# Kernel tuning notes

Measured on AMD Instinct MI355X. Metric: run time of the kernel, lower is better.

Reference implementation:

```python
import jax, jax.numpy as jnp
import numpy as np

N, IN_DIM, HID, HEADS, OUT_DIM = 4096, 512, 128, 4, 64
ALPHA = 0.2
NEG_INF = -9e15  # matches torch's -9000000000000000.0 fill


def _gat_layer(adj_mask, h, W, a, concat):
    # h: [N, Fin], W: [Fin, Fout], a: [2*Fout, 1]
    Wh = h @ W                                   # [N, Fout]
    f_out = W.shape[1]
    Wh1 = Wh @ a[:f_out]                         # [N, 1]
    Wh2 = Wh @ a[f_out:]                         # [N, 1]
    e = jax.nn.leaky_relu(Wh1 + Wh2.T, ALPHA)    # [N, N] broadcast scores
    e = jnp.where(adj_mask, e, NEG_INF)
    att = jax.nn.softmax(e, axis=1)              # masked row softmax
    out = att @ Wh                               # [N, Fout] aggregate
    return jax.nn.elu(out) if concat else out


def setup_inputs() -> dict:
    key = jax.random.key(0)
    k = jax.random.split(key, 6)
    g = jax.random.randint(k[0], (N, N), 0, 2, dtype=jnp.int32)
    inputs = jax.random.normal(k[1], (N, IN_DIM), dtype=jnp.float32)
    # xavier-uniform-like scales
    s1 = np.sqrt(6.0 / (IN_DIM + HID)) * 1.414
    sa1 = np.sqrt(6.0 / (2 * HID + 1)) * 1.414
    s2 = np.sqrt(6.0 / (HID * HEADS + OUT_DIM)) * 1.414
    sa2 = np.sqrt(6.0 / (2 * OUT_DIM + 1)) * 1.414
    W1 = jax.random.uniform(k[2], (HEADS, IN_DIM, HID), jnp.float32, -s1, s1)
    a1 = jax.random.uniform(k[3], (HEADS, 2 * HID, 1), jnp.float32, -sa1, sa1)
    W2 = jax.random.uniform(k[4], (HID * HEADS, OUT_DIM), jnp.float32, -s2, s2)
    a2 = jax.random.uniform(k[5], (2 * OUT_DIM, 1), jnp.float32, -sa2, sa2)
    return {"g": g, "inputs": inputs, "W1": W1, "a1": a1, "W2": W2, "a2": a2}


def reference(g, inputs, W1, a1, W2, a2):
    adj_mask = g > 0                                              # [N, N] bool
    # layer 1: HEADS parallel heads, concat=True (elu), then concat on features
    heads_out = jax.vmap(lambda W, a: _gat_layer(adj_mask, inputs, W, a, True))(W1, a1)
    h = jnp.transpose(heads_out, (1, 0, 2)).reshape(N, HEADS * HID)  # [N, H*HID]
    # output attention layer, concat=False (no elu)
    return _gat_layer(adj_mask, h, W2, a2, False)                 # [N, OUT_DIM]
```

## Files before the change

### kernel.cpp

```cpp
#include <hip/hip_runtime.h>
#include <hip/hip_bf16.h>
#include <stdint.h>

#define NN 4096
#define KD 512
#define LOG2E 1.4426950408889634f

typedef __attribute__((ext_vector_type(8))) short short8;
typedef __attribute__((ext_vector_type(4))) float f32x4;

__device__ __forceinline__ float lrelu(float x) { return fmaxf(x, 0.2f * x); }

__device__ __forceinline__ unsigned short f2bf(float f) {
    uint32_t u = __float_as_uint(f);
    u += 0x7fff + ((u >> 16) & 1);
    return (unsigned short)(u >> 16);
}

__device__ __forceinline__ float exp2_fast(float x) {
    float r; asm("v_exp_f32 %0, %1" : "=v"(r) : "v"(x)); return r;
}

__device__ __forceinline__ uint32_t cvt_pk_bf16(float lo, float hi) {
    uint32_t r; asm("v_cvt_pk_bf16_f32 %0, %1, %2" : "=v"(r) : "v"(lo), "v"(hi)); return r;
}

__device__ __forceinline__ void glds16(const void* g, void* l) {
    __builtin_amdgcn_global_load_lds(
        (const __attribute__((address_space(1))) uint32_t*)g,
        (__attribute__((address_space(3))) uint32_t*)l, 16, 0, 0);
}

__global__ void k_bitmask(const int* __restrict__ g, uint64_t* __restrict__ bm) {
    int wave = threadIdx.x >> 6;
    int lane = threadIdx.x & 63;
    int row = blockIdx.x * 4 + wave;
    const int* grow = g + (size_t)row * NN;
    for (int w = 0; w < 64; ++w) {
        int v = grow[w * 64 + lane];
        unsigned long long m = __ballot(v > 0);
        if (lane == 0) bm[(size_t)row * 64 + w] = m;
    }
}

__global__ void k_cast(const float* __restrict__ x, unsigned short* __restrict__ y, int n4) {
    int i = blockIdx.x * 256 + threadIdx.x;
    if (i < n4) {
        float4 v = ((const float4*)x)[i];
        uint2 o;
        o.x = (uint32_t)f2bf(v.x) | ((uint32_t)f2bf(v.y) << 16);
        o.y = (uint32_t)f2bf(v.z) | ((uint32_t)f2bf(v.w) << 16);
        ((uint2*)y)[i] = o;
    }
}

__global__ __launch_bounds__(256)
void k_tc(const float* __restrict__ src, unsigned short* __restrict__ dst, int R, int C) {
    __shared__ float tile[64][65];
    int b = blockIdx.z;
    int r0 = blockIdx.x * 64, c0 = blockIdx.y * 64;
    src += (size_t)b * R * C;
    dst += (size_t)b * C * R;
    int t = threadIdx.x;
    #pragma unroll
    for (int s = 0; s < 16; ++s) {
        int idx = t + s * 256;
        int r = idx >> 6, c = idx & 63;
        tile[r][c] = src[(size_t)(r0 + r) * C + c0 + c];
    }
    __syncthreads();
    #pragma unroll
    for (int s = 0; s < 16; ++s) {
        int idx = t + s * 256;
        int r = idx >> 6, c = idx & 63;
        dst[(size_t)(c0 + r) * R + r0 + c] = f2bf(tile[c][r]);
    }
}

template <int F>
__global__ __launch_bounds__(512)
void k_gemm_fused(const unsigned short* __restrict__ Abf, const unsigned short* __restrict__ WT,
                  const float* __restrict__ avec,
                  unsigned short* __restrict__ WhT, float* __restrict__ s1g,
                  float* __restrict__ s2g, unsigned int* __restrict__ smaxKey) {
    constexpr int BM = 32, BK = 64;
    constexpr int NCF = F / 64;
    __shared__ unsigned short a_lds[2][BM * BK];
    __shared__ unsigned short b_lds[2][F * BK];
    __shared__ unsigned short t_lds[F * 40];
    __shared__ float sred[BM][2];
    int t = threadIdx.x, lane = t & 63, w = t >> 6;
    int h = blockIdx.y;
    int i0 = blockIdx.x * BM;
    const unsigned short* WTh = WT + (size_t)h * F * KD;
    int r0 = (w >> 2) * 16, c0 = (w & 3) * (F / 4);
    int krow = lane & 15, kgrp = lane >> 4;
    if (t < BM) { sred[t][0] = 0.f; sred[t][1] = 0.f; }
    f32x4 acc[NCF];
    #pragma unroll
    for (int cf = 0; cf < NCF; ++cf) acc[cf] = (f32x4){0.f, 0.f, 0.f, 0.f};

    auto stage = [&](int buf, int kt) {
        int k0 = kt * BK;
        if (w < 4) {
            int c = w * 64 + lane;
            int row = c >> 3, slot = c & 7;
            glds16(Abf + (size_t)(i0 + row) * KD + k0 + ((slot ^ (row & 7)) * 8),
                   &a_lds[buf][(w * 64) * 8]);
        }
        #pragma unroll
        for (int s = 0; s < F / 64; ++s) {
            int c = w * F + s * 64 + lane;
            int row = c >> 3, slot = c & 7;
            glds16(WTh + (size_t)row * KD + k0 + ((slot ^ (row & 7)) * 8),
                   &b_lds[buf][(w * F + s * 64) * 8]);
        }
    };

    stage(0, 0);
    __syncthreads();
    int cur = 0;
    for (int kt = 0; kt < KD / BK; ++kt) {
        int nxt = cur ^ 1;
        if (kt + 1 < KD / BK) stage(nxt, kt + 1);
        #pragma unroll
        for (int ks = 0; ks < 2; ++ks) {
            int koff = ks * 32 + kgrp * 8;
            int arow = r0 + krow;
            short8 av = *(const short8*)((const char*)&a_lds[cur][arow * BK] +
                                         ((koff * 2) ^ ((arow & 7) << 4)));
            #pragma unroll
            for (int cf = 0; cf < NCF; ++cf) {
                int brow = c0 + cf * 16 + krow;
                short8 bv = *(const short8*)((const char*)&b_lds[cur][brow * BK] +
                                             ((koff * 2) ^ ((brow & 7) << 4)));
                acc[cf] = __builtin_amdgcn_mfma_f32_16x16x32_bf16(av, bv, acc[cf], 0, 0, 0);
            }
        }
        __syncthreads();
        cur = nxt;
    }
    float p1[4] = {0.f, 0.f, 0.f, 0.f}, p2[4] = {0.f, 0.f, 0.f, 0.f};
    const float* ah = avec + (size_t)h * 2 * F;
    #pragma unroll
    for (int cf = 0; cf < NCF; ++cf) {
        int col = c0 + cf * 16 + krow;
        float aw1 = ah[col], aw2 = ah[F + col];
        #pragma unroll
        for (int r = 0; r < 4; ++r) {
            int row = r0 + kgrp * 4 + r;
            t_lds[col * 40 + row] = f2bf(acc[cf][r]);
            p1[r] += acc[cf][r] * aw1;
            p2[r] += acc[cf][r] * aw2;
        }
    }
    #pragma unroll
    for (int d = 1; d < 16; d <<= 1) {
        #pragma unroll
        for (int r = 0; r < 4; ++r) { p1[r] += __shfl_xor(p1[r], d); p2[r] += __shfl_xor(p2[r], d); }
    }
    if (krow == 0) {
        #pragma unroll
        for (int r = 0; r < 4; ++r) {
            int row = r0 + kgrp * 4 + r;
            atomicAdd(&sred[row][0], p1[r]);
            atomicAdd(&sred[row][1], p2[r]);
        }
    }
    __syncthreads();
    {
        int col = t >> 2, seg = (t & 3) * 8;
        if (col < F) {
            uint4 v = *(const uint4*)&t_lds[col * 40 + seg];
            *(uint4*)&WhT[((size_t)h * F + col) * NN + i0 + seg] = v;
        }
    }
    if (t < BM) {
        s1g[(size_t)h * NN + i0 + t] = sred[t][0] * LOG2E;
        s2g[(size_t)h * NN + i0 + t] = sred[t][1] * LOG2E;
    }
    if (w == 0) {
        float v = (t < BM) ? sred[t][1] * LOG2E : -3.4e38f;
        #pragma unroll
        for (int d = 1; d < 64; d <<= 1) v = fmaxf(v, __shfl_xor(v, d));
        if (lane == 0) {
            uint32_t b = __float_as_uint(v);
            uint32_t key = (b & 0x80000000u) ? ~b : (b | 0x80000000u);
            atomicMax(smaxKey + h, key);
        }
    }
}

template <int F, int NW, int NJH>
__global__ __launch_bounds__(NW * 64, 4)
void k_agg3(const unsigned short* __restrict__ WhT, const float* __restrict__ s1v,
            const float* __restrict__ s2v, const unsigned int* __restrict__ smaxKey,
            const unsigned char* __restrict__ bmb,
            float* __restrict__ pnum, float* __restrict__ pden, int njt, int nh) {
    constexpr int TI = (NW / NJH) * 32, TJ = NJH * 32;
    constexpr int NB = F / 16;
    constexpr int TJ8 = TJ / 8;
    constexpr int CPR = TJ8;
    constexpr int CH_W = F * CPR / NW;
    constexpr int XF = F + 4;
    constexpr int XROWS = TI / 2;
    constexpr size_t ST_BYTES = sizeof(unsigned short) * 3 * F * TJ;
    constexpr size_t XCH_BYTES = sizeof(float) * (size_t)(NJH - 1) * XROWS * XF;
    constexpr size_t SM_BYTES = ST_BYTES > XCH_BYTES ? ST_BYTES : XCH_BYTES;
    __shared__ __align__(16) char smem[SM_BYTES];
    __shared__ float den_sh[NJH][TI];
    auto whT_lds = (unsigned short (*)[F * TJ])smem;
    float* xch = (float*)smem;
    int t = threadIdx.x, l = t & 63, w = t >> 6;
    int h = blockIdx.y, js = blockIdx.z;
    int i0 = blockIdx.x * TI;
    int rg = w / NJH, jh = w % NJH;
    int r0 = rg * 32;
    const unsigned short* WhTh = WhT + (size_t)h * F * NN;
    const float* s2h = s2v + (size_t)h * NN;
    unsigned int kk = smaxKey[h];
    float smax = __uint_as_float((kk & 0x80000000u) ? (kk ^ 0x80000000u) : ~kk);
    int rowA = i0 + r0 + (l & 15);
    int rowB = rowA + 16;
    float s1A = s1v[(size_t)h * NN + rowA];
    float s1B = s1v[(size_t)h * NN + rowB];
    float miA = lrelu(s1A + smax), miB = lrelu(s1B + smax);
    float c1A = s1A - miA, c2A = fmaf(0.2f, s1A, -miA);
    float c1B = s1B - miB, c2B = fmaf(0.2f, s1B, -miB);
    int kgrp = l >> 4;
    int joff = jh * 32 + kgrp * 8;
    int jsbase = js * njt;
    const unsigned char* bmbA = bmb + (size_t)rowA * 512;
    const unsigned char* bmbB = bmb + (size_t)rowB * 512;

    f32x4 acc[2][NB];
    #pragma unroll
    for (int m = 0; m < 2; ++m)
        #pragma unroll
        for (int b = 0; b < NB; ++b) acc[m][b] = (f32x4){0.f, 0.f, 0.f, 0.f};
    float denA = 0.f, denB = 0.f;

    struct SD { float4 q0, q1; unsigned int mA, mB; };
    struct PA { short8 a, b; };

    auto loadSD = [&](int jt) {
        SD s;
        int j0 = (jsbase + jt) * TJ;
        s.q0 = *(const float4*)&s2h[j0 + joff];
        s.q1 = *(const float4*)&s2h[j0 + joff + 4];
        int wb = (jsbase + jt) * CPR + jh * 4 + kgrp;
        s.mA = bmbA[wb];
        s.mB = bmbB[wb];
        return s;
    };

    auto computeP = [&](const SD& s) {
        float q[8] = {s.q0.x, s.q0.y, s.q0.z, s.q0.w, s.q1.x, s.q1.y, s.q1.z, s.q1.w};
        float pA[8], pB[8];
        #pragma unroll
        for (int u = 0; u < 8; ++u) {
            float tA = fmaxf(q[u] + c1A, fmaf(0.2f, q[u], c2A));
            float vA = ((s.mA >> u) & 1u) ? exp2_fast(tA) : 0.f;
            denA += vA; pA[u] = vA;
            float tB = fmaxf(q[u] + c1B, fmaf(0.2f, q[u], c2B));
            float vB = ((s.mB >> u) & 1u) ? exp2_fast(tB) : 0.f;
            denB += vB; pB[u] = vB;
        }
        union { uint32_t d[4]; short8 v; } ua, ub;
        #pragma unroll
        for (int j = 0; j < 4; ++j) {
            ua.d[j] = cvt_pk_bf16(pA[2 * j], pA[2 * j + 1]);
            ub.d[j] = cvt_pk_bf16(pB[2 * j], pB[2 * j + 1]);
        }
        PA p; p.a = ua.v; p.b = ub.v;
        return p;
    };

    auto stage = [&](int buf, int jt) {
        int j0 = (jsbase + jt) * TJ;
        #pragma unroll
        for (int s = 0; s < CH_W / 64; ++s) {
            int d = w * CH_W + s * 64 + l;
            int r = d & 15;
            int jsl = (d >> 4) & (TJ8 - 1);
            int b_ = d / (16 * TJ8);
            glds16(WhTh + (size_t)(b_ * 16 + r) * NN + j0 + jsl * 8,
                   &whT_lds[buf][(w * CH_W + s * 64) * 8]);
        }
    };

    auto domfma = [&](int buf, const PA& pa) {
        #pragma unroll
        for (int b = 0; b < NB; ++b) {
            int unit = (b * 16 + jh * 4 + kgrp) * 16 + (l & 15);
            short8 bv = *(const short8*)&whT_lds[buf][unit * 8];
            acc[0][b] = __builtin_amdgcn_mfma_f32_16x16x32_bf16(pa.a, bv, acc[0][b], 0, 0, 0);
            acc[1][b] = __builtin_amdgcn_mfma_f32_16x16x32_bf16(pa.b, bv, acc[1][b], 0, 0, 0);
        }
    };

    SD sd_cur = loadSD(0);
    __builtin_amdgcn_sched_barrier(0);
    stage(0, 0);
    __builtin_amdgcn_sched_barrier(0);
    SD sd_nxt;
    if (njt > 1) sd_nxt = loadSD(1);
    PA pa_cur = computeP(sd_cur);
    int cur = 0, nx1 = 1;
    for (int jt = 0; jt < njt; ++jt) {
        bool more = jt + 1 < njt;
        if (more) stage(nx1, jt + 1);
        __builtin_amdgcn_sched_barrier(0);
        SD sd2;
        if (jt + 2 < njt) sd2 = loadSD(jt + 2);
        PA pa_n;
        if (more) pa_n = computeP(sd_nxt);
        __builtin_amdgcn_sched_barrier(0);
        if (!more) asm volatile("s_waitcnt vmcnt(0)" ::: "memory");
        __builtin_amdgcn_s_barrier();
        __builtin_amdgcn_sched_barrier(0);
        domfma(cur, pa_cur);
        pa_cur = pa_n;
        sd_nxt = sd2;
        cur = nx1;
        nx1 = nx1 + 1 == 3 ? 0 : nx1 + 1;
    }

    denA += __shfl_xor(denA, 16); denA += __shfl_xor(denA, 32);
    denB += __shfl_xor(denB, 16); denB += __shfl_xor(denB, 32);
    if (l < 16) {
        den_sh[jh][r0 + l] = denA;
        den_sh[jh][r0 + 16 + l] = denB;
    }
    __syncthreads();

    float* pnumS = pnum + ((size_t)(js * nh + h) * NN + i0) * F;
    #pragma unroll
    for (int m = 0; m < 2; ++m) {
        if (jh > 0) {
            float* sl = xch + (size_t)(jh - 1) * XROWS * XF;
            #pragma unroll
            for (int b = 0; b < NB; ++b) {
                int col = b * 16 + (l & 15);
                #pragma unroll
                for (int r = 0; r < 4; ++r)
                    sl[(rg * 16 + (l >> 4) * 4 + r) * XF + col] = acc[m][b][r];
            }
        }
        __syncthreads();
        if (jh == 0) {
            #pragma unroll
            for (int b = 0; b < NB; ++b) {
                int col = b * 16 + (l & 15);
                #pragma unroll
                for (int r = 0; r < 4; ++r) {
                    int lrow = rg * 16 + (l >> 4) * 4 + r;
                    int row = r0 + m * 16 + (l >> 4) * 4 + r;
                    float v = acc[m][b][r];
                    #pragma unroll
                    for (int sX = 1; sX < NJH; ++sX)
                        v += xch[((size_t)(sX - 1) * XROWS + lrow) * XF + col];
                    pnumS[(size_t)row * F + col] = v;
                }
            }
        }
        __syncthreads();
    }
    if (t < TI) {
        float d = den_sh[0][t];
        #pragma unroll
        for (int sX = 1; sX < NJH; ++sX) d += den_sh[sX][t];
        pden[(size_t)(js * nh + h) * NN + i0 + t] = d;
    }
}

__global__ void k_reduce1(const float* __restrict__ pnum, const float* __restrict__ pden,
                          unsigned short* __restrict__ hbuf) {
    int idx = blockIdx.x * 256 + threadIdx.x;
    int i = idx >> 7;
    int c4 = idx & 127;
    int hh = c4 >> 5, f4 = c4 & 31;
    float4 a = *(const float4*)&pnum[((size_t)hh * NN + i) * 128 + f4 * 4];
    float4 b = *(const float4*)&pnum[((size_t)(4 + hh) * NN + i) * 128 + f4 * 4];
    float den = pden[(size_t)hh * NN + i] + pden[(size_t)(4 + hh) * NN + i];
    float inv = 1.f / den;
    float v[4] = {(a.x + b.x) * inv, (a.y + b.y) * inv, (a.z + b.z) * inv, (a.w + b.w) * inv};
    uint2 o;
    unsigned short e[4];
    #pragma unroll
    for (int u = 0; u < 4; ++u) {
        float x = v[u];
        x = x > 0.f ? x : expm1f(x);
        e[u] = f2bf(x);
    }
    o.x = (uint32_t)e[0] | ((uint32_t)e[1] << 16);
    o.y = (uint32_t)e[2] | ((uint32_t)e[3] << 16);
    *(uint2*)&hbuf[(size_t)i * 512 + c4 * 4] = o;
}

__global__ void k_reduce2(const float* __restrict__ pnum, const float* __restrict__ pden,
                          float* __restrict__ out) {
    int idx = blockIdx.x * 256 + threadIdx.x;
    int i = idx >> 4;
    int f4 = (idx & 15) * 4;
    float4 s = {0.f, 0.f, 0.f, 0.f};
    float den = 0.f;
    #pragma unroll
    for (int js = 0; js < 8; ++js) {
        float4 v = *(const float4*)&pnum[((size_t)js * NN + i) * 64 + f4];
        s.x += v.x; s.y += v.y; s.z += v.z; s.w += v.w;
        den += pden[(size_t)js * NN + i];
    }
    float inv = 1.f / den;
    s.x *= inv; s.y *= inv; s.z *= inv; s.w *= inv;
    *(float4*)&out[(size_t)i * 64 + f4] = s;
}

extern "C" void kernel_launch(void* const* d_in, const int* in_sizes, int n_in,
                              void* d_out, int out_size, void* d_ws, size_t ws_size,
                              hipStream_t stream) {
    const int*   g      = (const int*)d_in[0];
    const float* inputs = (const float*)d_in[1];
    const float* W1     = (const float*)d_in[2];
    const float* a1     = (const float*)d_in[3];
    const float* W2     = (const float*)d_in[4];
    const float* a2     = (const float*)d_in[5];
    float* out = (float*)d_out;
    char* ws = (char*)d_ws;

    size_t off = 0;
    uint64_t* bm   = (uint64_t*)(ws + off); off += (size_t)NN * 64 * 8;
    unsigned short* Xbf  = (unsigned short*)(ws + off); off += (size_t)NN * KD * 2;
    unsigned short* W1T  = (unsigned short*)(ws + off); off += (size_t)4 * 128 * KD * 2;
    unsigned short* W2T  = (unsigned short*)(ws + off); off += (size_t)64 * KD * 2;
    unsigned short* WhT1 = (unsigned short*)(ws + off); off += (size_t)4 * 128 * NN * 2;
    unsigned short* WhT2 = (unsigned short*)(ws + off); off += (size_t)64 * NN * 2;
    unsigned short* hbuf = (unsigned short*)(ws + off); off += (size_t)NN * KD * 2;
    float* s1_1    = (float*)(ws + off);    off += (size_t)4 * NN * 4;
    float* s2_1    = (float*)(ws + off);    off += (size_t)4 * NN * 4;
    float* s1_2    = (float*)(ws + off);    off += (size_t)NN * 4;
    float* s2_2    = (float*)(ws + off);    off += (size_t)NN * 4;
    unsigned int* keys = (unsigned int*)(ws + off); off += 256;
    float* pnum    = (float*)(ws + off);    off += (size_t)8 * NN * 128 * 4;
    float* pden    = (float*)(ws + off);    off += (size_t)8 * NN * 4;
    float* pnum2 = pnum;
    float* pden2 = pden;

    hipMemsetAsync(keys, 0, 32, stream);
    k_bitmask<<<NN / 4, 256, 0, stream>>>(g, bm);
    k_cast<<<(NN * KD / 4 + 255) / 256, 256, 0, stream>>>(inputs, Xbf, NN * KD / 4);
    k_tc<<<dim3(KD / 64, 2, 4), 256, 0, stream>>>(W1, W1T, KD, 128);
    k_tc<<<dim3(KD / 64, 1, 1), 256, 0, stream>>>(W2, W2T, KD, 64);
    k_gemm_fused<128><<<dim3(NN / 32, 4), 512, 0, stream>>>(Xbf, W1T, a1, WhT1, s1_1, s2_1, keys);
    k_agg3<128, 16, 4><<<dim3(NN / 128, 4, 2), 1024, 0, stream>>>(
        WhT1, s1_1, s2_1, keys, (const unsigned char*)bm, pnum, pden, NN / 128 / 2, 4);
    k_reduce1<<<NN * 128 / 256, 256, 0, stream>>>(pnum, pden, hbuf);
    k_gemm_fused<64><<<dim3(NN / 32, 1), 512, 0, stream>>>(hbuf, W2T, a2, WhT2, s1_2, s2_2, keys + 4);
    k_agg3<64, 8, 4><<<dim3(NN / 64, 1, 8), 512, 0, stream>>>(
        WhT2, s1_2, s2_2, keys + 4, (const unsigned char*)bm, pnum2, pden2, NN / 128 / 8, 1);
    k_reduce2<<<NN * 16 / 256, 256, 0, stream>>>(pnum2, pden2, out);
}
```

Measured before the change: 128.7 us.

## Restructure aggregation kernel pipeline to double buffering with smaller blocks

Replaces the triple-buffered LDS pipeline with double buffering. The MFMA work on the current tile now runs before the barrier, at raised wave priority, while the next tile is staged and its probabilities computed. Block sizes are halved for both attention layers, and the grid is flattened so head/split combos sit in the low bits of blockIdx.x, which interleaves them across CUs. The aim is more resident blocks, less LDS use and better overlap of loads with matrix math. The cost is a full vmcnt wait plus a barrier every iteration and less data reuse per block.

New measurement: 143.3 us. +11.4%, slower.

```diff
diff --git a/kernel.cpp b/kernel.cpp
--- a/kernel.cpp
+++ b/kernel.cpp
@@ -191,12 +191,13 @@
     }
 }
 
-template <int F, int NW, int NJH>
-__global__ __launch_bounds__(NW * 64, 4)
-void k_agg3(const unsigned short* __restrict__ WhT, const float* __restrict__ s1v,
+template <int F, int NW, int NJH, int MINW>
+__global__ __launch_bounds__(NW * 64, MINW)
+void k_agg5(const unsigned short* __restrict__ WhT, const float* __restrict__ s1v,
             const float* __restrict__ s2v, const unsigned int* __restrict__ smaxKey,
             const unsigned char* __restrict__ bmb,
-            float* __restrict__ pnum, float* __restrict__ pden, int njt, int nh) {
+            float* __restrict__ pnum, float* __restrict__ pden,
+            int njt, int nh, int njs) {
     constexpr int TI = (NW / NJH) * 32, TJ = NJH * 32;
     constexpr int NB = F / 16;
     constexpr int TJ8 = TJ / 8;
@@ -204,7 +205,7 @@
     constexpr int CH_W = F * CPR / NW;
     constexpr int XF = F + 4;
     constexpr int XROWS = TI / 2;
-    constexpr size_t ST_BYTES = sizeof(unsigned short) * 3 * F * TJ;
+    constexpr size_t ST_BYTES = sizeof(unsigned short) * 2 * F * TJ;
     constexpr size_t XCH_BYTES = sizeof(float) * (size_t)(NJH - 1) * XROWS * XF;
     constexpr size_t SM_BYTES = ST_BYTES > XCH_BYTES ? ST_BYTES : XCH_BYTES;
     __shared__ __align__(16) char smem[SM_BYTES];
@@ -212,22 +213,24 @@
     auto whT_lds = (unsigned short (*)[F * TJ])smem;
     float* xch = (float*)smem;
     int t = threadIdx.x, l = t & 63, w = t >> 6;
-    int h = blockIdx.y, js = blockIdx.z;
-    int i0 = blockIdx.x * TI;
+    int combo = blockIdx.x & 7;
+    int h = combo / njs;
+    int js = combo % njs;
+    int i0 = (int)(blockIdx.x >> 3) * TI;
     int rg = w / NJH, jh = w % NJH;
     int r0 = rg * 32;
     const unsigned short* WhTh = WhT + (size_t)h * F * NN;
     const float* s2h = s2v + (size_t)h * NN;
     unsigned int kk = smaxKey[h];
     float smax = __uint_as_float((kk & 0x80000000u) ? (kk ^ 0x80000000u) : ~kk);
-    int rowA = i0 + r0 + (l & 15);
+    int lane16 = l & 15, kgrp = l >> 4;
+    int rowA = i0 + r0 + lane16;
     int rowB = rowA + 16;
     float s1A = s1v[(size_t)h * NN + rowA];
     float s1B = s1v[(size_t)h * NN + rowB];
     float miA = lrelu(s1A + smax), miB = lrelu(s1B + smax);
     float c1A = s1A - miA, c2A = fmaf(0.2f, s1A, -miA);
     float c1B = s1B - miB, c2B = fmaf(0.2f, s1B, -miB);
-    int kgrp = l >> 4;
     int joff = jh * 32 + kgrp * 8;
     int jsbase = js * njt;
     const unsigned char* bmbA = bmb + (size_t)rowA * 512;
@@ -292,7 +295,7 @@
     auto domfma = [&](int buf, const PA& pa) {
         #pragma unroll
         for (int b = 0; b < NB; ++b) {
-            int unit = (b * 16 + jh * 4 + kgrp) * 16 + (l & 15);
+            int unit = (b * 16 + jh * 4 + kgrp) * 16 + lane16;
             short8 bv = *(const short8*)&whT_lds[buf][unit * 8];
             acc[0][b] = __builtin_amdgcn_mfma_f32_16x16x32_bf16(pa.a, bv, acc[0][b], 0, 0, 0);
             acc[1][b] = __builtin_amdgcn_mfma_f32_16x16x32_bf16(pa.b, bv, acc[1][b], 0, 0, 0);
@@ -306,24 +309,29 @@
     SD sd_nxt;
     if (njt > 1) sd_nxt = loadSD(1);
     PA pa_cur = computeP(sd_cur);
-    int cur = 0, nx1 = 1;
+    asm volatile("s_waitcnt vmcnt(0)" ::: "memory");
+    __builtin_amdgcn_s_barrier();
+    __builtin_amdgcn_sched_barrier(0);
+    int cur = 0;
     for (int jt = 0; jt < njt; ++jt) {
         bool more = jt + 1 < njt;
-        if (more) stage(nx1, jt + 1);
+        if (more) stage(cur ^ 1, jt + 1);
         __builtin_amdgcn_sched_barrier(0);
         SD sd2;
         if (jt + 2 < njt) sd2 = loadSD(jt + 2);
+        __builtin_amdgcn_s_setprio(1);
+        domfma(cur, pa_cur);
+        __builtin_amdgcn_s_setprio(0);
         PA pa_n;
         if (more) pa_n = computeP(sd_nxt);
-        __builtin_amdgcn_sched_barrier(0);
-        if (!more) asm volatile("s_waitcnt vmcnt(0)" ::: "memory");
-        __builtin_amdgcn_s_barrier();
-        __builtin_amdgcn_sched_barrier(0);
-        domfma(cur, pa_cur);
+        if (more) {
+            asm volatile("s_waitcnt vmcnt(0)" ::: "memory");
+            __builtin_amdgcn_s_barrier();
+            __builtin_amdgcn_sched_barrier(0);
+        }
         pa_cur = pa_n;
         sd_nxt = sd2;
-        cur = nx1;
-        nx1 = nx1 + 1 == 3 ? 0 : nx1 + 1;
+        cur ^= 1;
     }
 
     denA += __shfl_xor(denA, 16); denA += __shfl_xor(denA, 32);
@@ -341,21 +349,21 @@
             float* sl = xch + (size_t)(jh - 1) * XROWS * XF;
             #pragma unroll
             for (int b = 0; b < NB; ++b) {
-                int col = b * 16 + (l & 15);
+                int col = b * 16 + lane16;
                 #pragma unroll
                 for (int r = 0; r < 4; ++r)
-                    sl[(rg * 16 + (l >> 4) * 4 + r) * XF + col] = acc[m][b][r];
+                    sl[(rg * 16 + kgrp * 4 + r) * XF + col] = acc[m][b][r];
             }
         }
         __syncthreads();
         if (jh == 0) {
             #pragma unroll
             for (int b = 0; b < NB; ++b) {
-                int col = b * 16 + (l & 15);
+                int col = b * 16 + lane16;
                 #pragma unroll
                 for (int r = 0; r < 4; ++r) {
-                    int lrow = rg * 16 + (l >> 4) * 4 + r;
-                    int row = r0 + m * 16 + (l >> 4) * 4 + r;
+                    int lrow = rg * 16 + kgrp * 4 + r;
+                    int row = r0 + m * 16 + kgrp * 4 + r;
                     float v = acc[m][b][r];
                     #pragma unroll
                     for (int sX = 1; sX < NJH; ++sX)
@@ -452,11 +460,11 @@
     k_tc<<<dim3(KD / 64, 2, 4), 256, 0, stream>>>(W1, W1T, KD, 128);
     k_tc<<<dim3(KD / 64, 1, 1), 256, 0, stream>>>(W2, W2T, KD, 64);
     k_gemm_fused<128><<<dim3(NN / 32, 4), 512, 0, stream>>>(Xbf, W1T, a1, WhT1, s1_1, s2_1, keys);
-    k_agg3<128, 16, 4><<<dim3(NN / 128, 4, 2), 1024, 0, stream>>>(
-        WhT1, s1_1, s2_1, keys, (const unsigned char*)bm, pnum, pden, NN / 128 / 2, 4);
+    k_agg5<128, 8, 4, 4><<<(NN / 64) * 8, 512, 0, stream>>>(
+        WhT1, s1_1, s2_1, keys, (const unsigned char*)bm, pnum, pden, NN / 128 / 2, 4, 2);
     k_reduce1<<<NN * 128 / 256, 256, 0, stream>>>(pnum, pden, hbuf);
     k_gemm_fused<64><<<dim3(NN / 32, 1), 512, 0, stream>>>(hbuf, W2T, a2, WhT2, s1_2, s2_2, keys + 4);
-    k_agg3<64, 8, 4><<<dim3(NN / 64, 1, 8), 512, 0, stream>>>(
-        WhT2, s1_2, s2_2, keys + 4, (const unsigned char*)bm, pnum2, pden2, NN / 128 / 8, 1);
+    k_agg5<64, 4, 4, 4><<<(NN / 32) * 8, 256, 0, stream>>>(
+        WhT2, s1_2, s2_2, keys + 4, (const unsigned char*)bm, pnum2, pden2, NN / 128 / 8, 1, 8);
     k_reduce2<<<NN * 16 / 256, 256, 0, stream>>>(pnum2, pden2, out);
 }
```

## Factor masked softmax exponentials into per-column and per-row terms and swizzle WhT layout

Applied to the files above, without the earlier changes.

The attention weight exp2(lrelu(s1+s2) - m_i) is rewritten as the max of two products: a per-column exponential (precomputed once by a new k_prepE kernel) times a per-row constant. This removes all transcendental work from the aggregation inner loop, at the cost of two extra float loads per column group. WhT is also stored in 128-column blocks, and LDS staging uses an XOR swizzle on the j-group index to reduce bank conflicts on the B-operand reads. The bitmask loop gets an unroll pragma. The factorisation may lose a little precision, since products of separately rounded exponentials replace a single exp.

Result: slower. 212.8 us (+65.4%).

```diff
diff --git a/kernel.cpp b/kernel.cpp
--- a/kernel.cpp
+++ b/kernel.cpp
@@ -36,6 +36,7 @@
     int lane = threadIdx.x & 63;
     int row = blockIdx.x * 4 + wave;
     const int* grow = g + (size_t)row * NN;
+    #pragma unroll 4
     for (int w = 0; w < 64; ++w) {
         int v = grow[w * 64 + lane];
         unsigned long long m = __ballot(v > 0);
@@ -172,7 +173,8 @@
         int col = t >> 2, seg = (t & 3) * 8;
         if (col < F) {
             uint4 v = *(const uint4*)&t_lds[col * 40 + seg];
-            *(uint4*)&WhT[((size_t)h * F + col) * NN + i0 + seg] = v;
+            int jb = i0 >> 7, jl = (i0 & 127) + seg;
+            *(uint4*)&WhT[(((size_t)h * (NN / 128) + jb) * F + col) * 128 + jl] = v;
         }
     }
     if (t < BM) {
@@ -191,17 +193,29 @@
     }
 }
 
+__global__ void k_prepE(const float* __restrict__ s2, const unsigned int* __restrict__ keyp,
+                        float* __restrict__ e1, float* __restrict__ e2) {
+    int idx = blockIdx.x * 256 + threadIdx.x;
+    int h = idx >> 12;
+    unsigned int kk = keyp[h];
+    float smax = __uint_as_float((kk & 0x80000000u) ? (kk ^ 0x80000000u) : ~kk);
+    float d = s2[idx] - smax;
+    e1[idx] = exp2_fast(d);
+    e2[idx] = exp2_fast(0.2f * d);
+}
+
 template <int F, int NW, int NJH>
 __global__ __launch_bounds__(NW * 64, 4)
-void k_agg3(const unsigned short* __restrict__ WhT, const float* __restrict__ s1v,
-            const float* __restrict__ s2v, const unsigned int* __restrict__ smaxKey,
+void k_agg8(const unsigned short* __restrict__ WhT, const float* __restrict__ s1v,
+            const float* __restrict__ E1v, const float* __restrict__ E2v,
+            const unsigned int* __restrict__ smaxKey,
             const unsigned char* __restrict__ bmb,
             float* __restrict__ pnum, float* __restrict__ pden, int njt, int nh) {
     constexpr int TI = (NW / NJH) * 32, TJ = NJH * 32;
     constexpr int NB = F / 16;
-    constexpr int TJ8 = TJ / 8;
-    constexpr int CPR = TJ8;
-    constexpr int CH_W = F * CPR / NW;
+    constexpr int CPR = TJ / 8;
+    constexpr int TUNITS = F * (TJ / 8);
+    constexpr int CH_W = TUNITS / NW;
     constexpr int XF = F + 4;
     constexpr int XROWS = TI / 2;
     constexpr size_t ST_BYTES = sizeof(unsigned short) * 3 * F * TJ;
@@ -216,18 +230,19 @@
     int i0 = blockIdx.x * TI;
     int rg = w / NJH, jh = w % NJH;
     int r0 = rg * 32;
-    const unsigned short* WhTh = WhT + (size_t)h * F * NN;
-    const float* s2h = s2v + (size_t)h * NN;
+    const unsigned short* WhTt = WhT + (size_t)h * (NN / 128) * (F * 128);
+    const float* E1h = E1v + (size_t)h * NN;
+    const float* E2h = E2v + (size_t)h * NN;
     unsigned int kk = smaxKey[h];
     float smax = __uint_as_float((kk & 0x80000000u) ? (kk ^ 0x80000000u) : ~kk);
-    int rowA = i0 + r0 + (l & 15);
+    int lane16 = l & 15, kgrp = l >> 4;
+    int rowA = i0 + r0 + lane16;
     int rowB = rowA + 16;
     float s1A = s1v[(size_t)h * NN + rowA];
     float s1B = s1v[(size_t)h * NN + rowB];
-    float miA = lrelu(s1A + smax), miB = lrelu(s1B + smax);
-    float c1A = s1A - miA, c2A = fmaf(0.2f, s1A, -miA);
-    float c1B = s1B - miB, c2B = fmaf(0.2f, s1B, -miB);
-    int kgrp = l >> 4;
+    float zA = 0.8f * (s1A + smax), zB = 0.8f * (s1B + smax);
+    float K1A = exp2_fast(fminf(zA, 0.f)), K2A = exp2_fast(fminf(-zA, 0.f));
+    float K1B = exp2_fast(fminf(zB, 0.f)), K2B = exp2_fast(fminf(-zB, 0.f));
     int joff = jh * 32 + kgrp * 8;
     int jsbase = js * njt;
     const unsigned char* bmbA = bmb + (size_t)rowA * 512;
@@ -240,14 +255,16 @@
         for (int b = 0; b < NB; ++b) acc[m][b] = (f32x4){0.f, 0.f, 0.f, 0.f};
     float denA = 0.f, denB = 0.f;
 
-    struct SD { float4 q0, q1; unsigned int mA, mB; };
+    struct SD { float4 a0, a1, b0, b1; unsigned int mA, mB; };
     struct PA { short8 a, b; };
 
     auto loadSD = [&](int jt) {
         SD s;
         int j0 = (jsbase + jt) * TJ;
-        s.q0 = *(const float4*)&s2h[j0 + joff];
-        s.q1 = *(const float4*)&s2h[j0 + joff + 4];
+        s.a0 = *(const float4*)&E1h[j0 + joff];
+        s.a1 = *(const float4*)&E1h[j0 + joff + 4];
+        s.b0 = *(const float4*)&E2h[j0 + joff];
+        s.b1 = *(const float4*)&E2h[j0 + joff + 4];
         int wb = (jsbase + jt) * CPR + jh * 4 + kgrp;
         s.mA = bmbA[wb];
         s.mB = bmbB[wb];
@@ -255,15 +272,16 @@
     };
 
     auto computeP = [&](const SD& s) {
-        float q[8] = {s.q0.x, s.q0.y, s.q0.z, s.q0.w, s.q1.x, s.q1.y, s.q1.z, s.q1.w};
+        float e1v[8] = {s.a0.x, s.a0.y, s.a0.z, s.a0.w, s.a1.x, s.a1.y, s.a1.z, s.a1.w};
+        float e2v[8] = {s.b0.x, s.b0.y, s.b0.z, s.b0.w, s.b1.x, s.b1.y, s.b1.z, s.b1.w};
         float pA[8], pB[8];
         #pragma unroll
         for (int u = 0; u < 8; ++u) {
-            float tA = fmaxf(q[u] + c1A, fmaf(0.2f, q[u], c2A));
-            float vA = ((s.mA >> u) & 1u) ? exp2_fast(tA) : 0.f;
+            float vA = fmaxf(e1v[u] * K1A, e2v[u] * K2A);
+            vA = ((s.mA >> u) & 1u) ? vA : 0.f;
             denA += vA; pA[u] = vA;
-            float tB = fmaxf(q[u] + c1B, fmaf(0.2f, q[u], c2B));
-            float vB = ((s.mB >> u) & 1u) ? exp2_fast(tB) : 0.f;
+            float vB = fmaxf(e1v[u] * K1B, e2v[u] * K2B);
+            vB = ((s.mB >> u) & 1u) ? vB : 0.f;
             denB += vB; pB[u] = vB;
         }
         union { uint32_t d[4]; short8 v; } ua, ub;
@@ -277,22 +295,22 @@
     };
 
     auto stage = [&](int buf, int jt) {
-        int j0 = (jsbase + jt) * TJ;
+        const unsigned short* base = WhTt + (size_t)(jsbase + jt) * (F * 128);
         #pragma unroll
         for (int s = 0; s < CH_W / 64; ++s) {
-            int d = w * CH_W + s * 64 + l;
-            int r = d & 15;
-            int jsl = (d >> 4) & (TJ8 - 1);
-            int b_ = d / (16 * TJ8);
-            glds16(WhTh + (size_t)(b_ * 16 + r) * NN + j0 + jsl * 8,
-                   &whT_lds[buf][(w * CH_W + s * 64) * 8]);
+            int c = w * CH_W + s * 64 + l;
+            int f = c >> 4, jg = c & 15;
+            int srcu = f * 16 + (jg ^ (f & 7));
+            glds16(base + (size_t)srcu * 8, &whT_lds[buf][(w * CH_W + s * 64) * 8]);
         }
     };
 
     auto domfma = [&](int buf, const PA& pa) {
+        int joff2 = jh * 4 + kgrp;
         #pragma unroll
         for (int b = 0; b < NB; ++b) {
-            int unit = (b * 16 + jh * 4 + kgrp) * 16 + (l & 15);
+            int f = b * 16 + lane16;
+            int unit = f * 16 + (joff2 ^ (f & 7));
             short8 bv = *(const short8*)&whT_lds[buf][unit * 8];
             acc[0][b] = __builtin_amdgcn_mfma_f32_16x16x32_bf16(pa.a, bv, acc[0][b], 0, 0, 0);
             acc[1][b] = __builtin_amdgcn_mfma_f32_16x16x32_bf16(pa.b, bv, acc[1][b], 0, 0, 0);
@@ -341,21 +359,21 @@
             float* sl = xch + (size_t)(jh - 1) * XROWS * XF;
             #pragma unroll
             for (int b = 0; b < NB; ++b) {
-                int col = b * 16 + (l & 15);
+                int col = b * 16 + lane16;
                 #pragma unroll
                 for (int r = 0; r < 4; ++r)
-                    sl[(rg * 16 + (l >> 4) * 4 + r) * XF + col] = acc[m][b][r];
+                    sl[(rg * 16 + kgrp * 4 + r) * XF + col] = acc[m][b][r];
             }
         }
         __syncthreads();
         if (jh == 0) {
             #pragma unroll
             for (int b = 0; b < NB; ++b) {
-                int col = b * 16 + (l & 15);
+                int col = b * 16 + lane16;
                 #pragma unroll
                 for (int r = 0; r < 4; ++r) {
-                    int lrow = rg * 16 + (l >> 4) * 4 + r;
-                    int row = r0 + m * 16 + (l >> 4) * 4 + r;
+                    int lrow = rg * 16 + kgrp * 4 + r;
+                    int row = r0 + m * 16 + kgrp * 4 + r;
                     float v = acc[m][b][r];
                     #pragma unroll
                     for (int sX = 1; sX < NJH; ++sX)
@@ -440,6 +458,10 @@
     float* s2_1    = (float*)(ws + off);    off += (size_t)4 * NN * 4;
     float* s1_2    = (float*)(ws + off);    off += (size_t)NN * 4;
     float* s2_2    = (float*)(ws + off);    off += (size_t)NN * 4;
+    float* e1_1    = (float*)(ws + off);    off += (size_t)4 * NN * 4;
+    float* e2_1    = (float*)(ws + off);    off += (size_t)4 * NN * 4;
+    float* e1_2    = (float*)(ws + off);    off += (size_t)NN * 4;
+    float* e2_2    = (float*)(ws + off);    off += (size_t)NN * 4;
     unsigned int* keys = (unsigned int*)(ws + off); off += 256;
     float* pnum    = (float*)(ws + off);    off += (size_t)8 * NN * 128 * 4;
     float* pden    = (float*)(ws + off);    off += (size_t)8 * NN * 4;
@@ -452,11 +474,13 @@
     k_tc<<<dim3(KD / 64, 2, 4), 256, 0, stream>>>(W1, W1T, KD, 128);
     k_tc<<<dim3(KD / 64, 1, 1), 256, 0, stream>>>(W2, W2T, KD, 64);
     k_gemm_fused<128><<<dim3(NN / 32, 4), 512, 0, stream>>>(Xbf, W1T, a1, WhT1, s1_1, s2_1, keys);
-    k_agg3<128, 16, 4><<<dim3(NN / 128, 4, 2), 1024, 0, stream>>>(
-        WhT1, s1_1, s2_1, keys, (const unsigned char*)bm, pnum, pden, NN / 128 / 2, 4);
+    k_prepE<<<4 * NN / 256, 256, 0, stream>>>(s2_1, keys, e1_1, e2_1);
+    k_agg8<128, 16, 4><<<dim3(NN / 128, 4, 2), 1024, 0, stream>>>(
+        WhT1, s1_1, e1_1, e2_1, keys, (const unsigned char*)bm, pnum, pden, NN / 128 / 2, 4);
     k_reduce1<<<NN * 128 / 256, 256, 0, stream>>>(pnum, pden, hbuf);
     k_gemm_fused<64><<<dim3(NN / 32, 1), 512, 0, stream>>>(hbuf, W2T, a2, WhT2, s1_2, s2_2, keys + 4);
-    k_agg3<64, 8, 4><<<dim3(NN / 64, 1, 8), 512, 0, stream>>>(
-        WhT2, s1_2, s2_2, keys + 4, (const unsigned char*)bm, pnum2, pden2, NN / 128 / 8, 1);
+    k_prepE<<<NN / 256, 256, 0, stream>>>(s2_2, keys + 4, e1_2, e2_2);
+    k_agg8<64, 8, 4><<<dim3(NN / 64, 1, 8), 512, 0, stream>>>(
+        WhT2, s1_2, e1_2, e2_2, keys + 4, (const unsigned char*)bm, pnum2, pden2, NN / 128 / 8, 1);
     k_reduce2<<<NN * 16 / 256, 256, 0, stream>>>(pnum2, pden2, out);
 }
```

## Store WhT pre-tiled in LDS staging order for contiguous aggregation loads

Applied to the files above, without the earlier changes.

The fused GEMM epilogue now writes Wh transposed into 128-column tiles laid out in exactly the unit order the aggregation kernel stages into LDS. Each staging load becomes a contiguous 16-byte-per-lane copy of a tile instead of a strided gather across rows of length NN, which should improve coalescing and simplify address math. The bitmask loop also gets an unroll pragma. The producer now writes with scattered 16-byte stores, and the tiled layout assumes TJ equals 128 in both aggregation instantiations.

Measured after the change: 120.0 us. -6.8%, faster.

```diff
diff --git a/kernel.cpp b/kernel.cpp
--- a/kernel.cpp
+++ b/kernel.cpp
@@ -36,6 +36,7 @@
     int lane = threadIdx.x & 63;
     int row = blockIdx.x * 4 + wave;
     const int* grow = g + (size_t)row * NN;
+    #pragma unroll 4
     for (int w = 0; w < 64; ++w) {
         int v = grow[w * 64 + lane];
         unsigned long long m = __ballot(v > 0);
@@ -172,7 +173,9 @@
         int col = t >> 2, seg = (t & 3) * 8;
         if (col < F) {
             uint4 v = *(const uint4*)&t_lds[col * 40 + seg];
-            *(uint4*)&WhT[((size_t)h * F + col) * NN + i0 + seg] = v;
+            int jb = i0 >> 7, jl = (i0 & 127) + seg;
+            int unit = (col >> 4) * 256 + (jl >> 3) * 16 + (col & 15);
+            *(uint4*)&WhT[((size_t)h * (NN / 128) + jb) * ((size_t)F * 128) + (size_t)unit * 8] = v;
         }
     }
     if (t < BM) {
@@ -193,15 +196,15 @@
 
 template <int F, int NW, int NJH>
 __global__ __launch_bounds__(NW * 64, 4)
-void k_agg3(const unsigned short* __restrict__ WhT, const float* __restrict__ s1v,
-            const float* __restrict__ s2v, const unsigned int* __restrict__ smaxKey,
-            const unsigned char* __restrict__ bmb,
-            float* __restrict__ pnum, float* __restrict__ pden, int njt, int nh) {
+void k_agg10(const unsigned short* __restrict__ WhT, const float* __restrict__ s1v,
+             const float* __restrict__ s2v, const unsigned int* __restrict__ smaxKey,
+             const unsigned char* __restrict__ bmb,
+             float* __restrict__ pnum, float* __restrict__ pden, int njt, int nh) {
     constexpr int TI = (NW / NJH) * 32, TJ = NJH * 32;
     constexpr int NB = F / 16;
-    constexpr int TJ8 = TJ / 8;
-    constexpr int CPR = TJ8;
-    constexpr int CH_W = F * CPR / NW;
+    constexpr int CPR = TJ / 8;
+    constexpr int TUNITS = F * (TJ / 8);
+    constexpr int CH_W = TUNITS / NW;
     constexpr int XF = F + 4;
     constexpr int XROWS = TI / 2;
     constexpr size_t ST_BYTES = sizeof(unsigned short) * 3 * F * TJ;
@@ -216,18 +219,18 @@
     int i0 = blockIdx.x * TI;
     int rg = w / NJH, jh = w % NJH;
     int r0 = rg * 32;
-    const unsigned short* WhTh = WhT + (size_t)h * F * NN;
+    const unsigned short* WhTt = WhT + (size_t)h * (NN / 128) * ((size_t)F * 128);
     const float* s2h = s2v + (size_t)h * NN;
     unsigned int kk = smaxKey[h];
     float smax = __uint_as_float((kk & 0x80000000u) ? (kk ^ 0x80000000u) : ~kk);
-    int rowA = i0 + r0 + (l & 15);
+    int lane16 = l & 15, kgrp = l >> 4;
+    int rowA = i0 + r0 + lane16;
     int rowB = rowA + 16;
     float s1A = s1v[(size_t)h * NN + rowA];
     float s1B = s1v[(size_t)h * NN + rowB];
     float miA = lrelu(s1A + smax), miB = lrelu(s1B + smax);
     float c1A = s1A - miA, c2A = fmaf(0.2f, s1A, -miA);
     float c1B = s1B - miB, c2B = fmaf(0.2f, s1B, -miB);
-    int kgrp = l >> 4;
     int joff = jh * 32 + kgrp * 8;
     int jsbase = js * njt;
     const unsigned char* bmbA = bmb + (size_t)rowA * 512;
@@ -277,22 +280,18 @@
     };
 
     auto stage = [&](int buf, int jt) {
-        int j0 = (jsbase + jt) * TJ;
+        const unsigned short* base = WhTt + (size_t)(jsbase + jt) * ((size_t)F * 128);
         #pragma unroll
         for (int s = 0; s < CH_W / 64; ++s) {
-            int d = w * CH_W + s * 64 + l;
-            int r = d & 15;
-            int jsl = (d >> 4) & (TJ8 - 1);
-            int b_ = d / (16 * TJ8);
-            glds16(WhTh + (size_t)(b_ * 16 + r) * NN + j0 + jsl * 8,
-                   &whT_lds[buf][(w * CH_W + s * 64) * 8]);
+            int c0u = w * CH_W + s * 64;
+            glds16(base + (size_t)(c0u + l) * 8, &whT_lds[buf][c0u * 8]);
         }
     };
 
     auto domfma = [&](int buf, const PA& pa) {
         #pragma unroll
         for (int b = 0; b < NB; ++b) {
-            int unit = (b * 16 + jh * 4 + kgrp) * 16 + (l & 15);
+            int unit = (b * 16 + jh * 4 + kgrp) * 16 + lane16;
             short8 bv = *(const short8*)&whT_lds[buf][unit * 8];
             acc[0][b] = __builtin_amdgcn_mfma_f32_16x16x32_bf16(pa.a, bv, acc[0][b], 0, 0, 0);
             acc[1][b] = __builtin_amdgcn_mfma_f32_16x16x32_bf16(pa.b, bv, acc[1][b], 0, 0, 0);
@@ -341,21 +340,21 @@
             float* sl = xch + (size_t)(jh - 1) * XROWS * XF;
             #pragma unroll
             for (int b = 0; b < NB; ++b) {
-                int col = b * 16 + (l & 15);
+                int col = b * 16 + lane16;
                 #pragma unroll
                 for (int r = 0; r < 4; ++r)
-                    sl[(rg * 16 + (l >> 4) * 4 + r) * XF + col] = acc[m][b][r];
+                    sl[(rg * 16 + kgrp * 4 + r) * XF + col] = acc[m][b][r];
             }
         }
         __syncthreads();
         if (jh == 0) {
             #pragma unroll
             for (int b = 0; b < NB; ++b) {
-                int col = b * 16 + (l & 15);
+                int col = b * 16 + lane16;
                 #pragma unroll
                 for (int r = 0; r < 4; ++r) {
-                    int lrow = rg * 16 + (l >> 4) * 4 + r;
-                    int row = r0 + m * 16 + (l >> 4) * 4 + r;
+                    int lrow = rg * 16 + kgrp * 4 + r;
+                    int row = r0 + m * 16 + kgrp * 4 + r;
                     float v = acc[m][b][r];
                     #pragma unroll
                     for (int sX = 1; sX < NJH; ++sX)
@@ -452,11 +451,11 @@
     k_tc<<<dim3(KD / 64, 2, 4), 256, 0, stream>>>(W1, W1T, KD, 128);
     k_tc<<<dim3(KD / 64, 1, 1), 256, 0, stream>>>(W2, W2T, KD, 64);
     k_gemm_fused<128><<<dim3(NN / 32, 4), 512, 0, stream>>>(Xbf, W1T, a1, WhT1, s1_1, s2_1, keys);
-    k_agg3<128, 16, 4><<<dim3(NN / 128, 4, 2), 1024, 0, stream>>>(
+    k_agg10<128, 16, 4><<<dim3(NN / 128, 4, 2), 1024, 0, stream>>>(
         WhT1, s1_1, s2_1, keys, (const unsigned char*)bm, pnum, pden, NN / 128 / 2, 4);
     k_reduce1<<<NN * 128 / 256, 256, 0, stream>>>(pnum, pden, hbuf);
     k_gemm_fused<64><<<dim3(NN / 32, 1), 512, 0, stream>>>(hbuf, W2T, a2, WhT2, s1_2, s2_2, keys + 4);
-    k_agg3<64, 8, 4><<<dim3(NN / 64, 1, 8), 512, 0, stream>>>(
+    k_agg10<64, 8, 4><<<dim3(NN / 64, 1, 8), 512, 0, stream>>>(
         WhT2, s1_2, s2_2, keys + 4, (const unsigned char*)bm, pnum2, pden2, NN / 128 / 8, 1);
     k_reduce2<<<NN * 16 / 256, 256, 0, stream>>>(pnum2, pden2, out);
 }
```
